# Performance work log

Measured on AMD Instinct MI355X. Metric: run time of the kernel, lower is better.

## Reference

```python
import jax, jax.numpy as jnp
import numpy as np

B, N, DIM, DFF, CLS = 8, 1024, 768, 3072, 1

def setup_inputs() -> dict:
    key = jax.random.key(0)
    ks = jax.random.split(key, 12)
    x = jax.random.normal(ks[0], (B, N + CLS, DIM), dtype=jnp.float32)
    y = jax.random.normal(ks[1], (B, N + CLS, DIM), dtype=jnp.float32)
    coords = jax.random.uniform(ks[2], (N, N, 6), dtype=jnp.float32)
    U = jax.random.normal(ks[3], (DIM, DIM), dtype=jnp.float32) * (DIM ** -0.5)  # xavier-ish
    S1 = jax.random.uniform(ks[4], (DIM,), dtype=jnp.float32)
    S2 = jax.random.uniform(ks[5], (DIM,), dtype=jnp.float32)
    gating = jnp.asarray(1.0, dtype=jnp.float32)
    h_temp = jnp.asarray(0.1, dtype=jnp.float32)
    p_temp = jnp.asarray(1.0, dtype=jnp.float32)
    pos_emb = jax.random.uniform(ks[6], (N, 6, 1), dtype=jnp.float32)  # trunc_normal in [0,1]
    W1 = jax.random.normal(ks[7], (2 * DIM, DFF), dtype=jnp.float32) * 0.02
    b1 = jnp.zeros((DFF,), dtype=jnp.float32)
    W2 = jax.random.normal(ks[8], (DFF, DIM), dtype=jnp.float32) * 0.02
    b2 = jnp.zeros((DIM,), dtype=jnp.float32)
    return {"x": x, "y": y, "coords": coords, "U": U, "S1": S1, "S2": S2,
            "gating": gating, "h_temp": h_temp, "p_temp": p_temp, "pos_emb": pos_emb,
            "W1": W1, "b1": b1, "W2": W2, "b2": b2}

def reference(x, y, coords, U, S1, S2, gating, h_temp, p_temp, pos_emb, W1, b1, W2, b2):
    scale = DIM ** -0.5  # a_temp=False -> python float constant
    xb = x[:, CLS:, :]          # [B,N,D] (layer_norm=False -> Identity)
    yb = y[:, CLS:, :]
    y_cls = y[:, :CLS, :]
    # SpectralDecomp: x @ U.T @ diag(|S|) @ U, two spectra stacked -> [B,2,N,D]
    t = xb @ U.T
    xs = jnp.stack([(t * jnp.abs(S1)) @ U, (t * jnp.abs(S2)) @ U], axis=1)
    patch = jax.nn.softmax(jnp.einsum('bknd,bmd->bknm', xs, yb) * scale, axis=-1)  # [B,2,N,N]
    pos_logits = -jnp.abs(p_temp) * jnp.einsum('ijc,ic->ij', coords, pos_emb[..., 0])  # [N,N]
    pos = jax.nn.softmax(pos_logits, axis=-1)[None, None]  # broadcast to [B,2,N,N]
    g = jax.nn.sigmoid(gating)
    attn = (1.0 - g) * patch + g * pos  # [B,2,N,N]
    # entropy heat-map + hard routing
    entropy = jnp.sum(-attn * jnp.log(attn + 1e-8), axis=-1).transpose(0, 2, 1)  # [B,N,2]
    hmap = 2.0 - 2.0 * jax.nn.sigmoid(h_temp * entropy)
    fgbg = hmap[..., 0] >= hmap[..., 1]
    route = jnp.stack([fgbg, ~fgbg], axis=-1).astype(hmap.dtype)  # [B,N,2] one-hot
    heat_map = jnp.sum(hmap * route, axis=-1, keepdims=True)  # [B,N,1]
    attn_c = jnp.einsum('bkij,bik->bij', attn, route)  # route-weighted combine -> [B,N,N]
    y_out = attn_c @ yb  # [B,N,D]
    y_full = jnp.concatenate([y_cls, y_out], axis=1)  # [B,N+1,D]
    # proj MLP on concat(x, y)
    h = jnp.concatenate([x, y_full], axis=-1) @ W1 + b1
    xp = jax.nn.gelu(h, approximate=False) @ W2 + b2
    xp = jnp.concatenate([xp[:, :CLS], heat_map * xp[:, CLS:]], axis=1)
    return x + xp
```

## Files before the change

### kernel.cpp

```cpp
#include <hip/hip_runtime.h>
#include <hip/hip_bf16.h>
#include <math.h>

#define BB   8
#define NTOK 1024
#define DIM  768
#define DFF  3072
#define NP1  1025

typedef __bf16 bf16x8 __attribute__((ext_vector_type(8)));
typedef float  f32x4  __attribute__((ext_vector_type(4)));

__device__ __forceinline__ float waveMax(float v){
  #pragma unroll
  for (int o = 32; o > 0; o >>= 1) v = fmaxf(v, __shfl_down(v, o, 64));
  return v;
}
__device__ __forceinline__ float waveSum(float v){
  #pragma unroll
  for (int o = 32; o > 0; o >>= 1) v += __shfl_down(v, o, 64);
  return v;
}
__device__ __forceinline__ float blockMax(float v, float* red){
  int lane = threadIdx.x & 63, w = threadIdx.x >> 6;
  v = waveMax(v);
  if (lane == 0) red[w] = v;
  __syncthreads();
  float r = fmaxf(fmaxf(red[0], red[1]), fmaxf(red[2], red[3]));
  __syncthreads();
  return r;
}
__device__ __forceinline__ float blockSum(float v, float* red){
  int lane = threadIdx.x & 63, w = threadIdx.x >> 6;
  v = waveSum(v);
  if (lane == 0) red[w] = v;
  __syncthreads();
  float r = red[0] + red[1] + red[2] + red[3];
  __syncthreads();
  return r;
}

__global__ __launch_bounds__(256) void pos_kernel(
    const float* __restrict__ coords, const float* __restrict__ pos_emb,
    const float* __restrict__ p_temp, float* __restrict__ pos)
{
  int i = blockIdx.x;
  int tid = threadIdx.x;
  __shared__ float red[4];
  __shared__ float pe[6];
  if (tid < 6) pe[tid] = pos_emb[i*6 + tid];
  __syncthreads();
  float pt = fabsf(p_temp[0]);
  float v[4]; float mx = -INFINITY;
  #pragma unroll
  for (int j = 0; j < 4; j++){
    int jj = tid + j*256;
    const float* c = coords + ((long long)i*NTOK + jj)*6;
    float d = c[0]*pe[0] + c[1]*pe[1] + c[2]*pe[2] + c[3]*pe[3] + c[4]*pe[4] + c[5]*pe[5];
    v[j] = -pt * d;
    mx = fmaxf(mx, v[j]);
  }
  mx = blockMax(mx, red);
  float s = 0.f;
  #pragma unroll
  for (int j = 0; j < 4; j++){ v[j] = __expf(v[j] - mx); s += v[j]; }
  s = blockSum(s, red);
  float inv = 1.f / s;
  #pragma unroll
  for (int j = 0; j < 4; j++) pos[(long long)i*NTOK + tid + j*256] = v[j] * inv;
}

__global__ __launch_bounds__(256) void rowproc_kernel(
    const float* __restrict__ S,
    const float* __restrict__ pos,
    __hip_bfloat16* __restrict__ attnc,
    float* __restrict__ heat,
    const float* __restrict__ gating, const float* __restrict__ h_temp)
{
  int row = blockIdx.x;
  int b = row >> 10, i = row & 1023;
  int tid = threadIdx.x;
  __shared__ __align__(16) float a0[NTOK];
  __shared__ __align__(16) float a1[NTOK];
  __shared__ float red[4];
  float g = 1.f / (1.f + __expf(-gating[0]));
  float ht = h_temp[0];
  float ent[2];
  const int c0 = tid * 4;
  f32x4 pv = *(const f32x4*)&pos[(long long)i*NTOK + c0];
  #pragma unroll
  for (int k = 0; k < 2; k++){
    const float* Sr = S + ((long long)((k*8 + b)*NTOK) + i) * NTOK;
    f32x4 v = *(const f32x4*)&Sr[c0];
    float mx = fmaxf(fmaxf(v[0], v[1]), fmaxf(v[2], v[3]));
    mx = blockMax(mx, red);
    float s = 0.f;
    #pragma unroll
    for (int j = 0; j < 4; j++){ v[j] = __expf(v[j] - mx); s += v[j]; }
    s = blockSum(s, red);
    float inv = 1.f / s;
    float e = 0.f;
    float* arow = k ? a1 : a0;
    f32x4 at;
    #pragma unroll
    for (int j = 0; j < 4; j++){
      at[j] = (1.f - g) * (v[j] * inv) + g * pv[j];
      e += -at[j] * __logf(at[j] + 1e-8f);
    }
    *(f32x4*)&arow[c0] = at;
    ent[k] = blockSum(e, red);
  }
  float h0 = 2.f - 2.f / (1.f + __expf(-ht * ent[0]));
  float h1 = 2.f - 2.f / (1.f + __expf(-ht * ent[1]));
  bool fg = (h0 >= h1);
  if (tid == 0) heat[row] = fg ? h0 : h1;
  const float* sel = fg ? a0 : a1;
  f32x4 sv = *(const f32x4*)&sel[c0];
  union { __hip_bfloat16 h[4]; uint2 u; } pk;
  #pragma unroll
  for (int j = 0; j < 4; j++) pk.h[j] = __float2bfloat16(sv[j]);
  *(uint2*)(attnc + ((long long)b*NTOK + i)*NTOK + c0) = pk.u;
}

__global__ __launch_bounds__(256) void conv_xy_kernel(
    const float* __restrict__ x, const float* __restrict__ y, __hip_bfloat16* __restrict__ xy)
{
  long long idx = (long long)blockIdx.x*256 + threadIdx.x;
  int d = (int)(idx % DIM);
  long long br = idx / DIM;
  int r = (int)(br % NP1);
  xy[br*1536 + d] = __float2bfloat16(x[idx]);
  if (r == 0) xy[br*1536 + DIM + d] = __float2bfloat16(y[idx]);
}

__global__ __launch_bounds__(256) void transpose_conv_kernel(
    const float* __restrict__ in, long long sIn, int ldin,
    __hip_bfloat16* __restrict__ outT, long long sT,
    __hip_bfloat16* __restrict__ outS, long long sS,
    int R, int C,
    const float* __restrict__ sc1, const float* __restrict__ sc2,
    __hip_bfloat16* __restrict__ outT1, __hip_bfloat16* __restrict__ outT2)
{
  __shared__ float tile[32][33];
  int bx = blockIdx.x, by = blockIdx.y, z = blockIdx.z;
  const float* inb = in + (long long)z*sIn;
  int tx = threadIdx.x & 31, ty = threadIdx.x >> 5;
  #pragma unroll
  for (int p = 0; p < 4; p++){
    int r = by*32 + p*8 + ty;
    int c = bx*32 + tx;
    float v = inb[(long long)r*ldin + c];
    tile[p*8 + ty][tx] = v;
    if (outS) outS[(long long)z*sS + (long long)r*C + c] = __float2bfloat16(v);
  }
  __syncthreads();
  #pragma unroll
  for (int p = 0; p < 4; p++){
    int c = bx*32 + p*8 + ty;
    int r = by*32 + tx;
    float v = tile[tx][p*8 + ty];
    long long oidx = (long long)z*sT + (long long)c*R + r;
    outT[oidx] = __float2bfloat16(v);
    if (outT1) outT1[(long long)c*R + r] = __float2bfloat16(v * fabsf(sc1[r]));
    if (outT2) outT2[(long long)c*R + r] = __float2bfloat16(v * fabsf(sc2[r]));
  }
}

__device__ __forceinline__ void async16(const __bf16* gp, __bf16* lp){
  __builtin_amdgcn_global_load_lds(
      (const __attribute__((address_space(1))) void*)gp,
      (__attribute__((address_space(3))) void*)lp, 16, 0, 0);
}

template<int EPI>
__global__ __launch_bounds__(256) void mfma_gemm(
    const __bf16* __restrict__ A, const __bf16* __restrict__ Bm, void* __restrict__ Cv,
    int M, int N, int K, int lda, int ldb, int ldc,
    long long sAz, long long sBz, long long sCz,
    int maskA, int shiftB, int maskB, float alpha,
    const float* __restrict__ bias,
    const float* __restrict__ xres,
    const float* __restrict__ heat)
{
  __shared__ __align__(16) __bf16 Atile[128*32];
  __shared__ __align__(16) __bf16 Btile[128*32];

  const int tid  = threadIdx.x;
  const int lane = tid & 63;
  const int wv   = tid >> 6;
  const int wr   = wv >> 1, wc = wv & 1;
  const int n0 = blockIdx.x * 128, m0 = blockIdx.y * 128;
  const int z  = blockIdx.z;

  const __bf16* Ab = A  + (long long)(z & maskA) * sAz;
  const __bf16* Bb = Bm + (long long)((z >> shiftB) & maskB) * sBz;

  const int fr_row = lane & 15;
  const int fr_k   = (lane >> 4) * 8;

  f32x4 acc[4][4] = {};

  for (int k0 = 0; k0 < K; k0 += 32){
    __syncthreads();
    #pragma unroll
    for (int i = 0; i < 2; i++){
      int s   = wv*128 + i*64 + lane;
      int row = s >> 2;
      int kc  = (s & 3) * 8;
      int gm = m0 + row; if (gm > M-1) gm = M-1;
      int gn = n0 + row; if (gn > N-1) gn = N-1;
      async16(Ab + (long long)gm*lda + (k0 + kc), &Atile[(wv*128 + i*64)*8]);
      async16(Bb + (long long)gn*ldb + (k0 + kc), &Btile[(wv*128 + i*64)*8]);
    }
    __syncthreads();
    bf16x8 af[4], bfv[4];
    #pragma unroll
    for (int r = 0; r < 4; r++)
      af[r] = *(const bf16x8*)&Atile[(wr*64 + r*16 + fr_row)*32 + fr_k];
    #pragma unroll
    for (int c = 0; c < 4; c++)
      bfv[c] = *(const bf16x8*)&Btile[(wc*64 + c*16 + fr_row)*32 + fr_k];
    #pragma unroll
    for (int r = 0; r < 4; r++)
      #pragma unroll
      for (int c = 0; c < 4; c++)
        acc[r][c] = __builtin_amdgcn_mfma_f32_16x16x32_bf16(af[r], bfv[c], acc[r][c], 0, 0, 0);
  }

  const int col_l = lane & 15;
  const int row_l = (lane >> 4) * 4;
  #pragma unroll
  for (int r = 0; r < 4; r++){
    #pragma unroll
    for (int c = 0; c < 4; c++){
      int gn  = n0 + wc*64 + c*16 + col_l;
      int gm0 = m0 + wr*64 + r*16 + row_l;
      if (gn >= N) continue;
      f32x4 v = acc[r][c];
      #pragma unroll
      for (int reg = 0; reg < 4; reg++){
        int gm = gm0 + reg;
        if (gm >= M) continue;
        float cval = v[reg];
        long long cidx = (long long)z*sCz + (long long)gm*ldc + gn;
        if (EPI == 0){
          ((float*)Cv)[cidx] = alpha * cval;
        } else if (EPI == 1){
          ((__hip_bfloat16*)Cv)[cidx] = __float2bfloat16(cval);
        } else if (EPI == 2){
          float h = cval + bias[gn];
          float ge = 0.5f * h * (1.f + erff(h * 0.70710678118654752f));
          ((__hip_bfloat16*)Cv)[cidx] = __float2bfloat16(ge);
        } else {
          float h = cval + bias[gn];
          int bq = gm / NP1;
          int rr = gm - bq * NP1;
          float f = (rr == 0) ? 1.f : heat[bq*NTOK + (rr - 1)];
          ((float*)Cv)[cidx] = xres[cidx] + f * h;
        }
      }
    }
  }
}

extern "C" void kernel_launch(void* const* d_in, const int* in_sizes, int n_in,
                              void* d_out, int out_size, void* d_ws, size_t ws_size,
                              hipStream_t stream)
{
  const float* x       = (const float*)d_in[0];
  const float* y       = (const float*)d_in[1];
  const float* coords  = (const float*)d_in[2];
  const float* U       = (const float*)d_in[3];
  const float* S1      = (const float*)d_in[4];
  const float* S2      = (const float*)d_in[5];
  const float* gating  = (const float*)d_in[6];
  const float* h_temp  = (const float*)d_in[7];
  const float* p_temp  = (const float*)d_in[8];
  const float* pos_emb = (const float*)d_in[9];
  const float* W1      = (const float*)d_in[10];
  const float* b1      = (const float*)d_in[11];
  const float* W2      = (const float*)d_in[12];
  const float* b2      = (const float*)d_in[13];
  float* out = (float*)d_out;
  char* ws = (char*)d_ws;

  size_t off = 0;
  auto alloc = [&](size_t bytes){ size_t r = off; off = (off + bytes + 255) & ~(size_t)255; return r; };
  const long long NN  = (long long)NTOK * NTOK;
  const long long DD  = (long long)DIM * DIM;
  const size_t o_pos  = alloc(NN * 4);
  const size_t o_S    = alloc((size_t)2*BB*NN * 4);
  const size_t o_xy   = alloc((size_t)BB*NP1*1536 * 2);
  const size_t o_yb   = alloc((size_t)BB*NTOK*DIM * 2);
  const size_t o_ybT  = alloc((size_t)BB*DIM*NTOK * 2);
  const size_t o_xs   = alloc((size_t)2*BB*NTOK*DIM * 2);
  const size_t o_attn = alloc((size_t)BB*NN * 2);
  const size_t o_UT   = alloc((size_t)DD * 2);
  const size_t o_UTs  = alloc((size_t)2*DD * 2);
  const size_t o_Mk   = alloc((size_t)2*DD * 2);
  const size_t o_W1T  = alloc((size_t)DFF*2*DIM * 2);
  const size_t o_W2T  = alloc((size_t)DIM*DFF * 2);
  const size_t o_heat = alloc((size_t)BB*NTOK * 4);

  float*  S_f  = (float*)(ws + o_S);
  __hip_bfloat16* hg   = (__hip_bfloat16*)(ws + o_S);
  __hip_bfloat16* xy   = (__hip_bfloat16*)(ws + o_xy);
  __hip_bfloat16* yb   = (__hip_bfloat16*)(ws + o_yb);
  __hip_bfloat16* ybT  = (__hip_bfloat16*)(ws + o_ybT);
  __hip_bfloat16* xs   = (__hip_bfloat16*)(ws + o_xs);
  __hip_bfloat16* attnc= (__hip_bfloat16*)(ws + o_attn);
  __hip_bfloat16* UT   = (__hip_bfloat16*)(ws + o_UT);
  __hip_bfloat16* UTs  = (__hip_bfloat16*)(ws + o_UTs);
  __hip_bfloat16* Mk   = (__hip_bfloat16*)(ws + o_Mk);
  __hip_bfloat16* W1T  = (__hip_bfloat16*)(ws + o_W1T);
  __hip_bfloat16* W2T  = (__hip_bfloat16*)(ws + o_W2T);
  float* pos  = (float*)(ws + o_pos);
  float* heat = (float*)(ws + o_heat);

  const float scale = 0.03608439182435161f;
  dim3 blk(256);

  pos_kernel<<<dim3(NTOK), blk, 0, stream>>>(coords, pos_emb, p_temp, pos);
  conv_xy_kernel<<<dim3((BB*NP1*DIM)/256), blk, 0, stream>>>(x, y, xy);
  transpose_conv_kernel<<<dim3(DIM/32, DIM/32, 1), blk, 0, stream>>>(
      U, 0LL, DIM, UT, 0LL, nullptr, 0LL, DIM, DIM, S1, S2, UTs, UTs + DD);
  transpose_conv_kernel<<<dim3(DFF/32, (2*DIM)/32, 1), blk, 0, stream>>>(
      W1, 0LL, DFF, W1T, 0LL, nullptr, 0LL, 2*DIM, DFF, nullptr, nullptr, nullptr, nullptr);
  transpose_conv_kernel<<<dim3(DIM/32, DFF/32, 1), blk, 0, stream>>>(
      W2, 0LL, DIM, W2T, 0LL, nullptr, 0LL, DFF, DIM, nullptr, nullptr, nullptr, nullptr);
  transpose_conv_kernel<<<dim3(DIM/32, NTOK/32, BB), blk, 0, stream>>>(
      y + DIM, (long long)NP1*DIM, DIM, ybT, (long long)DIM*NTOK, yb, (long long)NTOK*DIM,
      NTOK, DIM, nullptr, nullptr, nullptr, nullptr);

  mfma_gemm<1><<<dim3(DIM/128, DIM/128, 2), blk, 0, stream>>>(
      (const __bf16*)UT, (const __bf16*)UTs, Mk,
      DIM, DIM, DIM, DIM, DIM, DIM,
      0LL, DD, DD, 0, 0, 1, 1.f, nullptr, nullptr, nullptr);

  mfma_gemm<1><<<dim3(DIM/128, NTOK/128, 16), blk, 0, stream>>>(
      (const __bf16*)(xy + 1536), (const __bf16*)Mk, xs,
      NTOK, DIM, DIM, 1536, DIM, DIM,
      (long long)NP1*1536, DD, (long long)NTOK*DIM,
      7, 3, 1, 1.f, nullptr, nullptr, nullptr);

  mfma_gemm<0><<<dim3(NTOK/128, NTOK/128, 16), blk, 0, stream>>>(
      (const __bf16*)xs, (const __bf16*)yb, S_f,
      NTOK, NTOK, DIM, DIM, DIM, NTOK,
      (long long)NTOK*DIM, (long long)NTOK*DIM, NN,
      15, 0, 7, scale, nullptr, nullptr, nullptr);

  rowproc_kernel<<<dim3(BB*NTOK), blk, 0, stream>>>(S_f, pos, attnc, heat, gating, h_temp);

  mfma_gemm<1><<<dim3(DIM/128, NTOK/128, BB), blk, 0, stream>>>(
      (const __bf16*)attnc, (const __bf16*)ybT, xy + 1536 + DIM,
      NTOK, DIM, NTOK, NTOK, NTOK, 1536,
      NN, (long long)DIM*NTOK, (long long)NP1*1536,
      7, 0, 7, 1.f, nullptr, nullptr, nullptr);

  mfma_gemm<2><<<dim3(DFF/128, (BB*NP1 + 127)/128, 1), blk, 0, stream>>>(
      (const __bf16*)xy, (const __bf16*)W1T, hg,
      BB*NP1, DFF, 2*DIM, 1536, 1536, DFF,
      0LL, 0LL, 0LL, 0, 0, 0, 1.f, b1, nullptr, nullptr);

  mfma_gemm<3><<<dim3(DIM/128, (BB*NP1 + 127)/128, 1), blk, 0, stream>>>(
      (const __bf16*)hg, (const __bf16*)W2T, out,
      BB*NP1, DIM, DFF, DFF, DFF, DIM,
      0LL, 0LL, 0LL, 0, 0, 0, 1.f, b2, x, heat);
}
```

Before: 619.2 us.

## Switch GEMM to 32x32x16 MFMA with swizzled LDS and store attention logits in bf16

The GEMM kernel now uses 32x32x16 bf16 MFMA instructions with 2x2 accumulators per wave instead of 4x4 16x16 tiles. It precomputes global and LDS pointers, and XOR-swizzles the LDS k-chunk layout to cut bank conflicts. The attention-logit GEMM now writes bf16 instead of fp32, roughly halving S traffic into the row-softmax kernel. The bf16 logits lose precision before the softmax and entropy routing, which could flip hard fg/bg routing decisions.

```diff
diff --git a/kernel.cpp b/kernel.cpp
--- a/kernel.cpp
+++ b/kernel.cpp
@@ -10,6 +10,7 @@
 
 typedef __bf16 bf16x8 __attribute__((ext_vector_type(8)));
 typedef float  f32x4  __attribute__((ext_vector_type(4)));
+typedef float  f32x16 __attribute__((ext_vector_type(16)));
 
 __device__ __forceinline__ float waveMax(float v){
   #pragma unroll
@@ -71,7 +72,7 @@
 }
 
 __global__ __launch_bounds__(256) void rowproc_kernel(
-    const float* __restrict__ S,
+    const __hip_bfloat16* __restrict__ S,
     const float* __restrict__ pos,
     __hip_bfloat16* __restrict__ attnc,
     float* __restrict__ heat,
@@ -90,8 +91,12 @@
   f32x4 pv = *(const f32x4*)&pos[(long long)i*NTOK + c0];
   #pragma unroll
   for (int k = 0; k < 2; k++){
-    const float* Sr = S + ((long long)((k*8 + b)*NTOK) + i) * NTOK;
-    f32x4 v = *(const f32x4*)&Sr[c0];
+    const __hip_bfloat16* Sr = S + ((long long)((k*8 + b)*NTOK) + i) * NTOK;
+    union { uint2 u; __hip_bfloat16 h[4]; } ld;
+    ld.u = *(const uint2*)&Sr[c0];
+    f32x4 v;
+    #pragma unroll
+    for (int j = 0; j < 4; j++) v[j] = __bfloat162float(ld.h[j]);
     float mx = fmaxf(fmaxf(v[0], v[1]), fmaxf(v[2], v[3]));
     mx = blockMax(mx, red);
     float s = 0.f;
@@ -195,68 +200,92 @@
   const __bf16* Ab = A  + (long long)(z & maskA) * sAz;
   const __bf16* Bb = Bm + (long long)((z >> shiftB) & maskB) * sBz;
 
-  const int fr_row = lane & 15;
-  const int fr_k   = (lane >> 4) * 8;
-
-  f32x4 acc[4][4] = {};
+  const __bf16* gA[2]; const __bf16* gB[2];
+  #pragma unroll
+  for (int i = 0; i < 2; i++){
+    int s   = wv*128 + i*64 + lane;
+    int row = s >> 2;
+    int kc  = (s & 3) ^ ((row >> 1) & 3);
+    int gm = m0 + row; if (gm > M-1) gm = M-1;
+    int gn = n0 + row; if (gn > N-1) gn = N-1;
+    gA[i] = Ab + (long long)gm * lda + kc * 8;
+    gB[i] = Bb + (long long)gn * ldb + kc * 8;
+  }
+  __bf16* ldsA0 = &Atile[(wv*128      ) * 8];
+  __bf16* ldsA1 = &Atile[(wv*128 + 64 ) * 8];
+  __bf16* ldsB0 = &Btile[(wv*128      ) * 8];
+  __bf16* ldsB1 = &Btile[(wv*128 + 64 ) * 8];
+
+  const int fm = lane & 31;
+  const int kq = lane >> 5;
+  const int sw = (fm >> 1) & 3;
+  const __bf16* pA[2][2]; const __bf16* pB[2][2];
+  #pragma unroll
+  for (int rr = 0; rr < 2; rr++)
+    #pragma unroll
+    for (int kh = 0; kh < 2; kh++){
+      int rowA = wr*64 + rr*32 + fm;
+      int rowB = wc*64 + rr*32 + fm;
+      pA[rr][kh] = &Atile[(rowA*4 + ((kh*2 + kq) ^ sw)) * 8];
+      pB[rr][kh] = &Btile[(rowB*4 + ((kh*2 + kq) ^ sw)) * 8];
+    }
+
+  f32x16 acc[2][2] = {};
 
   for (int k0 = 0; k0 < K; k0 += 32){
     __syncthreads();
-    #pragma unroll
-    for (int i = 0; i < 2; i++){
-      int s   = wv*128 + i*64 + lane;
-      int row = s >> 2;
-      int kc  = (s & 3) * 8;
-      int gm = m0 + row; if (gm > M-1) gm = M-1;
-      int gn = n0 + row; if (gn > N-1) gn = N-1;
-      async16(Ab + (long long)gm*lda + (k0 + kc), &Atile[(wv*128 + i*64)*8]);
-      async16(Bb + (long long)gn*ldb + (k0 + kc), &Btile[(wv*128 + i*64)*8]);
-    }
+    async16(gA[0], ldsA0); async16(gA[1], ldsA1);
+    async16(gB[0], ldsB0); async16(gB[1], ldsB1);
+    gA[0] += 32; gA[1] += 32; gB[0] += 32; gB[1] += 32;
     __syncthreads();
-    bf16x8 af[4], bfv[4];
-    #pragma unroll
-    for (int r = 0; r < 4; r++)
-      af[r] = *(const bf16x8*)&Atile[(wr*64 + r*16 + fr_row)*32 + fr_k];
-    #pragma unroll
-    for (int c = 0; c < 4; c++)
-      bfv[c] = *(const bf16x8*)&Btile[(wc*64 + c*16 + fr_row)*32 + fr_k];
-    #pragma unroll
-    for (int r = 0; r < 4; r++)
+    bf16x8 af[2][2], bfv[2][2];
+    #pragma unroll
+    for (int rr = 0; rr < 2; rr++)
       #pragma unroll
-      for (int c = 0; c < 4; c++)
-        acc[r][c] = __builtin_amdgcn_mfma_f32_16x16x32_bf16(af[r], bfv[c], acc[r][c], 0, 0, 0);
-  }
-
-  const int col_l = lane & 15;
-  const int row_l = (lane >> 4) * 4;
-  #pragma unroll
-  for (int r = 0; r < 4; r++){
-    #pragma unroll
-    for (int c = 0; c < 4; c++){
-      int gn  = n0 + wc*64 + c*16 + col_l;
-      int gm0 = m0 + wr*64 + r*16 + row_l;
+      for (int kh = 0; kh < 2; kh++){
+        af [rr][kh] = *(const bf16x8*)pA[rr][kh];
+        bfv[rr][kh] = *(const bf16x8*)pB[rr][kh];
+      }
+    #pragma unroll
+    for (int r = 0; r < 2; r++)
+      #pragma unroll
+      for (int c = 0; c < 2; c++){
+        acc[r][c] = __builtin_amdgcn_mfma_f32_32x32x16_bf16(af[r][0], bfv[c][0], acc[r][c], 0, 0, 0);
+        acc[r][c] = __builtin_amdgcn_mfma_f32_32x32x16_bf16(af[r][1], bfv[c][1], acc[r][c], 0, 0, 0);
+      }
+  }
+
+  const int col_l = lane & 31;
+  const int row_q = (lane >> 5) * 4;
+  #pragma unroll
+  for (int r = 0; r < 2; r++){
+    #pragma unroll
+    for (int c = 0; c < 2; c++){
+      int gn  = n0 + wc*64 + c*32 + col_l;
       if (gn >= N) continue;
-      f32x4 v = acc[r][c];
+      int gmb = m0 + wr*64 + r*32 + row_q;
+      f32x16 v = acc[r][c];
       #pragma unroll
-      for (int reg = 0; reg < 4; reg++){
-        int gm = gm0 + reg;
-        if (gm >= M) continue;
-        float cval = v[reg];
-        long long cidx = (long long)z*sCz + (long long)gm*ldc + gn;
-        if (EPI == 0){
-          ((float*)Cv)[cidx] = alpha * cval;
-        } else if (EPI == 1){
-          ((__hip_bfloat16*)Cv)[cidx] = __float2bfloat16(cval);
-        } else if (EPI == 2){
-          float h = cval + bias[gn];
-          float ge = 0.5f * h * (1.f + erff(h * 0.70710678118654752f));
-          ((__hip_bfloat16*)Cv)[cidx] = __float2bfloat16(ge);
-        } else {
-          float h = cval + bias[gn];
-          int bq = gm / NP1;
-          int rr = gm - bq * NP1;
-          float f = (rr == 0) ? 1.f : heat[bq*NTOK + (rr - 1)];
-          ((float*)Cv)[cidx] = xres[cidx] + f * h;
+      for (int g = 0; g < 4; g++){
+        #pragma unroll
+        for (int q = 0; q < 4; q++){
+          int gm = gmb + g*8 + q;
+          if (gm >= M) continue;
+          float cval = alpha * v[g*4 + q];
+          long long cidx = (long long)z*sCz + (long long)gm*ldc + gn;
+          if (EPI == 1){
+            ((__hip_bfloat16*)Cv)[cidx] = __float2bfloat16(cval);
+          } else if (EPI == 2){
+            float h = cval + bias[gn];
+            float ge = 0.5f * h * (1.f + erff(h * 0.70710678118654752f));
+            ((__hip_bfloat16*)Cv)[cidx] = __float2bfloat16(ge);
+          } else {
+            float h = cval + bias[gn];
+            int bq = gm / NP1;
+            int rr2 = gm - bq * NP1;
+            float f = (rr2 == 0) ? 1.f : heat[bq*NTOK + (rr2 - 1)];
+            ((float*)Cv)[cidx] = xres[cidx] + f * h;
+          }
         }
       }
     }
@@ -289,7 +318,7 @@
   const long long NN  = (long long)NTOK * NTOK;
   const long long DD  = (long long)DIM * DIM;
   const size_t o_pos  = alloc(NN * 4);
-  const size_t o_S    = alloc((size_t)2*BB*NN * 4);
+  const size_t o_S    = alloc((size_t)BB*NP1*DFF * 2);
   const size_t o_xy   = alloc((size_t)BB*NP1*1536 * 2);
   const size_t o_yb   = alloc((size_t)BB*NTOK*DIM * 2);
   const size_t o_ybT  = alloc((size_t)BB*DIM*NTOK * 2);
@@ -302,7 +331,7 @@
   const size_t o_W2T  = alloc((size_t)DIM*DFF * 2);
   const size_t o_heat = alloc((size_t)BB*NTOK * 4);
 
-  float*  S_f  = (float*)(ws + o_S);
+  __hip_bfloat16* S_bf = (__hip_bfloat16*)(ws + o_S);
   __hip_bfloat16* hg   = (__hip_bfloat16*)(ws + o_S);
   __hip_bfloat16* xy   = (__hip_bfloat16*)(ws + o_xy);
   __hip_bfloat16* yb   = (__hip_bfloat16*)(ws + o_yb);
@@ -343,13 +372,13 @@
       (long long)NP1*1536, DD, (long long)NTOK*DIM,
       7, 3, 1, 1.f, nullptr, nullptr, nullptr);
 
-  mfma_gemm<0><<<dim3(NTOK/128, NTOK/128, 16), blk, 0, stream>>>(
-      (const __bf16*)xs, (const __bf16*)yb, S_f,
+  mfma_gemm<1><<<dim3(NTOK/128, NTOK/128, 16), blk, 0, stream>>>(
+      (const __bf16*)xs, (const __bf16*)yb, S_bf,
       NTOK, NTOK, DIM, DIM, DIM, NTOK,
       (long long)NTOK*DIM, (long long)NTOK*DIM, NN,
       15, 0, 7, scale, nullptr, nullptr, nullptr);
 
-  rowproc_kernel<<<dim3(BB*NTOK), blk, 0, stream>>>(S_f, pos, attnc, heat, gating, h_temp);
+  rowproc_kernel<<<dim3(BB*NTOK), blk, 0, stream>>>(S_bf, pos, attnc, heat, gating, h_temp);
 
   mfma_gemm<1><<<dim3(DIM/128, NTOK/128, BB), blk, 0, stream>>>(
       (const __bf16*)attnc, (const __bf16*)ybT, xy + 1536 + DIM,
```

Result: faster. 579.0 us (-6.5%).
